# Optimization experiments

Hardware: AMD Instinct MI355X
Metric: run time of the kernel (lower is better)

Reference implementation:

```python
import jax, jax.numpy as jnp
import numpy as np
import math

B, L, C = 8, 1024, 256
H, CH = 8, 32  # num_heads, c_hidden; H*CH == C


def setup_inputs() -> dict:
    key = jax.random.key(0)
    ks = jax.random.split(key, 8)
    s = 0.02
    return {
        "q_x": jax.random.normal(ks[0], (B, L, C), jnp.float32),
        "bias_mask": jnp.zeros((B, 1, 1, L), jnp.float32),
        "bias_pair": jax.random.normal(ks[1], (B, H, L, L), jnp.float32),
        "Wq": jax.random.normal(ks[2], (C, H * CH), jnp.float32) * s,
        "Wk": jax.random.normal(ks[3], (C, H * CH), jnp.float32) * s,
        "Wv": jax.random.normal(ks[4], (C, H * CH), jnp.float32) * s,
        "Wg": jax.random.normal(ks[5], (C, H * CH), jnp.float32) * s,
        "bg": jnp.ones((H * CH,), jnp.float32),  # gating bias init = 1 in AlphaFold
        "Wo": jax.random.normal(ks[6], (H * CH, C), jnp.float32) * s,
        "bo": jnp.zeros((C,), jnp.float32),
    }


def reference(q_x, bias_mask, bias_pair, Wq, Wk, Wv, Wg, bg, Wo, bo):
    # QKV projections (self-attention: kv_x = q_x), split heads -> [B, H, L, CH]
    def proj(W):
        return (q_x @ W).reshape(B, L, H, CH).transpose(0, 2, 1, 3)

    q = proj(Wq) / math.sqrt(CH)
    k = proj(Wk)
    v = proj(Wv)

    # scores + multi-bias add, stable softmax over keys
    a = jnp.einsum("bhqc,bhkc->bhqk", q, k) + bias_mask + bias_pair
    a = jax.nn.softmax(a, axis=-1)

    # weighted values -> [B, L, H, CH]
    o = jnp.einsum("bhqk,bhkc->bhqc", a, v).transpose(0, 2, 1, 3)

    # sigmoid gating from query data
    g = jax.nn.sigmoid(q_x @ Wg + bg).reshape(B, L, H, CH)
    o = o * g

    # merge heads and output projection
    o = o.reshape(B, L, H * CH)
    return o @ Wo + bo
```

## Files before the change

kernel.cpp:

```cpp
#include <hip/hip_runtime.h>
#include <hip/hip_bf16.h>
#include <hip/hip_fp16.h>
#include <math.h>

#define BB 8
#define LL 1024
#define CC 256
#define HH 8
#define CHD 32

typedef __attribute__((ext_vector_type(8))) _Float16 half8;
typedef __attribute__((ext_vector_type(4))) float f32x4;
typedef __attribute__((ext_vector_type(4))) unsigned int u32x4;

__device__ __forceinline__ float u2f(unsigned short u) {
    return __uint_as_float(((unsigned)u) << 16);
}

__device__ __forceinline__ float ldv(const void* p, size_t i, bool f32) {
    return f32 ? ((const float*)p)[i] : u2f(((const unsigned short*)p)[i]);
}
__device__ __forceinline__ float4 ldv4(const void* p, size_t i, bool f32) {
    if (f32) return *(const float4*)((const float*)p + i);
    ushort4 u = *(const ushort4*)((const unsigned short*)p + i);
    return make_float4(u2f(u.x), u2f(u.y), u2f(u.z), u2f(u.w));
}
__device__ __forceinline__ bool probe_f32(const void* bg) {
    return *(const unsigned*)bg == 0x3F800000u;
}

__device__ __forceinline__ unsigned pack_h2(float a, float b) {
    __half2 h = __floats2half2_rn(a, b);
    return *(unsigned*)&h;
}

__global__ __launch_bounds__(256) void proj_kernel(
    const void* __restrict__ qx,
    const void* __restrict__ Wq, const void* __restrict__ Wk,
    const void* __restrict__ Wv, const void* __restrict__ Wg,
    const void* __restrict__ bg,
    __half* __restrict__ q_ws, __half* __restrict__ k_ws,
    __half* __restrict__ vt_ws, __half* __restrict__ g_ws)
{
    const bool f32 = probe_f32(bg);
    __shared__ __align__(16) float xs[16][256];
    const int t  = threadIdx.x;
    const int r0 = blockIdx.x * 16;

    {
        float4* dst = (float4*)(&xs[0][0]);
        for (int i = t; i < 1024; i += 256)
            dst[i] = ldv4(qx, (size_t)r0 * CC + (size_t)i * 4, f32);
    }
    __syncthreads();

    const int mat = t >> 6;
    const int c0  = (t & 63) << 2;
    const void* W = (mat == 0) ? Wq : (mat == 1) ? Wk : (mat == 2) ? Wv : Wg;

    float acc[16][4];
#pragma unroll
    for (int r = 0; r < 16; ++r)
#pragma unroll
        for (int j = 0; j < 4; ++j) acc[r][j] = 0.f;

    for (int kc = 0; kc < 64; ++kc) {
        float4 w[4];
#pragma unroll
        for (int i = 0; i < 4; ++i)
            w[i] = ldv4(W, (size_t)(4 * kc + i) * 256 + c0, f32);
#pragma unroll
        for (int r = 0; r < 16; ++r) {
            float4 x4 = *(const float4*)(&xs[r][kc * 4]);
            acc[r][0] += x4.x * w[0].x + x4.y * w[1].x + x4.z * w[2].x + x4.w * w[3].x;
            acc[r][1] += x4.x * w[0].y + x4.y * w[1].y + x4.z * w[2].y + x4.w * w[3].y;
            acc[r][2] += x4.x * w[0].z + x4.y * w[1].z + x4.z * w[2].z + x4.w * w[3].z;
            acc[r][3] += x4.x * w[0].w + x4.y * w[1].w + x4.z * w[2].w + x4.w * w[3].w;
        }
    }

    if (mat == 3) {
        float bgv[4];
#pragma unroll
        for (int j = 0; j < 4; ++j) bgv[j] = ldv(bg, c0 + j, f32);
#pragma unroll
        for (int r = 0; r < 16; ++r) {
            const int row = r0 + r;
#pragma unroll
            for (int j = 0; j < 4; ++j) {
                float z = acc[r][j] + bgv[j];
                float g = 1.f / (1.f + __expf(-z));
                g_ws[(size_t)row * 256 + c0 + j] = __float2half(g);
            }
        }
    } else if (mat == 2) {
        const int bI = r0 >> 10, l0 = r0 & 1023;
#pragma unroll
        for (int j = 0; j < 4; ++j) {
            const int col = c0 + j, hh = col >> 5, ch = col & 31;
            __half* dst = vt_ws + ((size_t)(bI * HH + hh) * CHD + ch) * LL + l0;
            unsigned p[8];
#pragma unroll
            for (int u = 0; u < 8; ++u)
                p[u] = pack_h2(acc[2 * u][j], acc[2 * u + 1][j]);
            u32x4 w0 = {p[0], p[1], p[2], p[3]};
            u32x4 w1 = {p[4], p[5], p[6], p[7]};
            *(u32x4*)dst = w0;
            *((u32x4*)dst + 1) = w1;
        }
    } else {
        const float scale = (mat == 0) ? 0.17677669529663687f : 1.f;
        __half* dst = (mat == 0) ? q_ws : k_ws;
#pragma unroll
        for (int r = 0; r < 16; ++r) {
            const int row = r0 + r;
            const int b = row >> 10, l = row & 1023;
#pragma unroll
            for (int j = 0; j < 4; ++j) {
                const int col = c0 + j;
                const int h = col >> 5, ch = col & 31;
                dst[((size_t)(b * HH + h) * LL + l) * CHD + ch] =
                    __float2half(acc[r][j] * scale);
            }
        }
    }
}

__global__ __launch_bounds__(256) void attn_mfma_kernel(
    const __half* __restrict__ q_ws, const __half* __restrict__ k_ws,
    const __half* __restrict__ vt_ws, const __half* __restrict__ g_ws,
    const void* __restrict__ mask, const void* __restrict__ bias,
    const void* __restrict__ bg,
    float* __restrict__ og_out)
{
    const bool f32 = probe_f32(bg);
    const int t  = threadIdx.x;
    const int wv = t >> 6;
    const int ln = t & 63;
    const int lq = ln & 15;
    const int g  = ln >> 4;
    const int bh = blockIdx.y;
    const int b  = bh >> 3, h = bh & 7;
    const int q0 = blockIdx.x * 64 + wv * 16;
    const int qi = q0 + lq;

    const half8 qfrag = *(const half8*)(q_ws + ((size_t)bh * LL + qi) * CHD + 8 * g);

    f32x4 o0 = {0.f, 0.f, 0.f, 0.f};
    f32x4 o1 = {0.f, 0.f, 0.f, 0.f};
    float m_run = -1e30f, l_run = 0.f;

    const size_t bias_base = ((size_t)bh * LL + qi) * LL;
    const size_t mask_base = (size_t)b * LL;
    const f32x4 zz = {0.f, 0.f, 0.f, 0.f};

    for (int k0 = 0; k0 < LL; k0 += 64) {
        f32x4 sc[4];
#pragma unroll
        for (int s = 0; s < 4; ++s) {
            half8 kf = *(const half8*)(k_ws +
                ((size_t)bh * LL + k0 + 16 * s + lq) * CHD + 8 * g);
            sc[s] = __builtin_amdgcn_mfma_f32_16x16x32_f16(kf, qfrag, zz, 0, 0, 0);
        }
#pragma unroll
        for (int s = 0; s < 4; ++s) {
            const int kk = k0 + 16 * s + 4 * g;
            float4 b4 = ldv4(bias, bias_base + kk, f32);
            float4 m4 = ldv4(mask, mask_base + kk, f32);
            sc[s].x += b4.x + m4.x;
            sc[s].y += b4.y + m4.y;
            sc[s].z += b4.z + m4.z;
            sc[s].w += b4.w + m4.w;
        }
        float mt = fmaxf(fmaxf(sc[0].x, sc[0].y), fmaxf(sc[0].z, sc[0].w));
#pragma unroll
        for (int s = 1; s < 4; ++s)
            mt = fmaxf(mt, fmaxf(fmaxf(sc[s].x, sc[s].y), fmaxf(sc[s].z, sc[s].w)));
        mt = fmaxf(mt, __shfl_xor(mt, 16));
        mt = fmaxf(mt, __shfl_xor(mt, 32));
        const float mn = fmaxf(m_run, mt);
        const float alpha = __expf(m_run - mn);
        m_run = mn;
        float ls = 0.f;
#pragma unroll
        for (int s = 0; s < 4; ++s) {
            sc[s].x = __expf(sc[s].x - mn); ls += sc[s].x;
            sc[s].y = __expf(sc[s].y - mn); ls += sc[s].y;
            sc[s].z = __expf(sc[s].z - mn); ls += sc[s].z;
            sc[s].w = __expf(sc[s].w - mn); ls += sc[s].w;
        }
        ls += __shfl_xor(ls, 16);
        ls += __shfl_xor(ls, 32);
        l_run = l_run * alpha + ls;
        o0 = o0 * alpha;
        o1 = o1 * alpha;

        unsigned ph[4][2];
#pragma unroll
        for (int s = 0; s < 4; ++s) {
            ph[s][0] = pack_h2(sc[s].x, sc[s].y);
            ph[s][1] = pack_h2(sc[s].z, sc[s].w);
        }
#pragma unroll
        for (int tt = 0; tt < 2; ++tt) {
            unsigned bfr[4];
#pragma unroll
            for (int w = 0; w < 4; ++w) {
                const int src = lq + 16 * (2 * (g & 1) + (w >> 1));
                unsigned lo = (unsigned)__shfl((int)ph[2 * tt + 0][w & 1], src);
                unsigned hi = (unsigned)__shfl((int)ph[2 * tt + 1][w & 1], src);
                bfr[w] = (g >= 2) ? hi : lo;
            }
            u32x4 bv = {bfr[0], bfr[1], bfr[2], bfr[3]};
            half8 pB = __builtin_bit_cast(half8, bv);
            half8 vf0 = *(const half8*)(vt_ws +
                ((size_t)bh * CHD + lq) * LL + k0 + 32 * tt + 8 * g);
            o0 = __builtin_amdgcn_mfma_f32_16x16x32_f16(vf0, pB, o0, 0, 0, 0);
            half8 vf1 = *(const half8*)(vt_ws +
                ((size_t)bh * CHD + 16 + lq) * LL + k0 + 32 * tt + 8 * g);
            o1 = __builtin_amdgcn_mfma_f32_16x16x32_f16(vf1, pB, o1, 0, 0, 0);
        }
    }

    const float inv = 1.f / l_run;
    const size_t row = (size_t)b * LL + qi;
    const __half* gp = g_ws + row * CC + h * CHD + 4 * g;
    float* op = og_out + row * CC + h * CHD + 4 * g;
    float4 r0, r1;
    r0.x = o0.x * inv * __half2float(gp[0]);
    r0.y = o0.y * inv * __half2float(gp[1]);
    r0.z = o0.z * inv * __half2float(gp[2]);
    r0.w = o0.w * inv * __half2float(gp[3]);
    r1.x = o1.x * inv * __half2float(gp[16]);
    r1.y = o1.y * inv * __half2float(gp[17]);
    r1.z = o1.z * inv * __half2float(gp[18]);
    r1.w = o1.w * inv * __half2float(gp[19]);
    *(float4*)op = r0;
    *(float4*)(op + 16) = r1;
}

__global__ __launch_bounds__(256) void out_kernel(
    float* __restrict__ io,
    const void* __restrict__ Wo, const void* __restrict__ bo,
    const void* __restrict__ bg)
{
    const bool f32 = probe_f32(bg);
    __shared__ __align__(16) float xs[16][256];
    const int t  = threadIdx.x;
    const int r0 = blockIdx.x * 16;
    {
        const float4* src = (const float4*)(io + (size_t)r0 * CC);
        float4* dst = (float4*)(&xs[0][0]);
        for (int i = t; i < 1024; i += 256) dst[i] = src[i];
    }
    __syncthreads();

    float acc[16];
#pragma unroll
    for (int r = 0; r < 16; ++r) acc[r] = 0.f;

    for (int kc = 0; kc < 64; ++kc) {
        const float w0 = ldv(Wo, (size_t)(4 * kc + 0) * 256 + t, f32);
        const float w1 = ldv(Wo, (size_t)(4 * kc + 1) * 256 + t, f32);
        const float w2 = ldv(Wo, (size_t)(4 * kc + 2) * 256 + t, f32);
        const float w3 = ldv(Wo, (size_t)(4 * kc + 3) * 256 + t, f32);
#pragma unroll
        for (int r = 0; r < 16; ++r) {
            float4 x4 = *(const float4*)(&xs[r][kc * 4]);
            acc[r] += x4.x * w0 + x4.y * w1 + x4.z * w2 + x4.w * w3;
        }
    }
    const float bov = ldv(bo, t, f32);
#pragma unroll
    for (int r = 0; r < 16; ++r)
        io[(size_t)(r0 + r) * CC + t] = acc[r] + bov;
}

extern "C" void kernel_launch(void* const* d_in, const int* in_sizes, int n_in,
                              void* d_out, int out_size, void* d_ws, size_t ws_size,
                              hipStream_t stream) {
    const void* qx   = d_in[0];
    const void* mask = d_in[1];
    const void* bias = d_in[2];
    const void* Wq   = d_in[3];
    const void* Wk   = d_in[4];
    const void* Wv   = d_in[5];
    const void* Wg   = d_in[6];
    const void* bg   = d_in[7];
    const void* Wo   = d_in[8];
    const void* bo   = d_in[9];
    float* out = (float*)d_out;

    char* ws = (char*)d_ws;
    const size_t TEN = (size_t)BB * LL * CC * sizeof(__half);
    __half* q_ws  = (__half*)(ws + 0 * TEN);
    __half* k_ws  = (__half*)(ws + 1 * TEN);
    __half* vt_ws = (__half*)(ws + 2 * TEN);
    __half* g_ws  = (__half*)(ws + 3 * TEN);

    proj_kernel<<<dim3(512), 256, 0, stream>>>(qx, Wq, Wk, Wv, Wg, bg,
                                               q_ws, k_ws, vt_ws, g_ws);
    attn_mfma_kernel<<<dim3(16, 64), 256, 0, stream>>>(q_ws, k_ws, vt_ws, g_ws,
                                                       mask, bias, bg, out);
    out_kernel<<<dim3(512), 256, 0, stream>>>(out, Wo, bo, bg);
}
```

Baseline: 546.0 us.

## Move QKVG and output projections onto fp16 MFMA with hi/lo split precision

```diff
diff --git a/kernel.cpp b/kernel.cpp
--- a/kernel.cpp
+++ b/kernel.cpp
@@ -13,10 +13,13 @@
 typedef __attribute__((ext_vector_type(4))) float f32x4;
 typedef __attribute__((ext_vector_type(4))) unsigned int u32x4;
 
+#define MFMA16 __builtin_amdgcn_mfma_f32_16x16x32_f16
+#define LO_SCALE 2048.f
+#define LO_INV   4.8828125e-4f
+
 __device__ __forceinline__ float u2f(unsigned short u) {
     return __uint_as_float(((unsigned)u) << 16);
 }
-
 __device__ __forceinline__ float ldv(const void* p, size_t i, bool f32) {
     return f32 ? ((const float*)p)[i] : u2f(((const unsigned short*)p)[i]);
 }
@@ -28,100 +31,148 @@
 __device__ __forceinline__ bool probe_f32(const void* bg) {
     return *(const unsigned*)bg == 0x3F800000u;
 }
-
 __device__ __forceinline__ unsigned pack_h2(float a, float b) {
     __half2 h = __floats2half2_rn(a, b);
     return *(unsigned*)&h;
 }
-
-__global__ __launch_bounds__(256) void proj_kernel(
-    const void* __restrict__ qx,
+__device__ __forceinline__ void store_h4(__half* p, float a, float b, float c, float d) {
+    uint2 u = make_uint2(pack_h2(a, b), pack_h2(c, d));
+    *(uint2*)p = u;
+}
+__device__ __forceinline__ void cvt_store_hilo(__half* ph, __half* pl, float4 v) {
+    __half2 a = __floats2half2_rn(v.x, v.y), b2 = __floats2half2_rn(v.z, v.w);
+    *(uint2*)ph = make_uint2(*(unsigned*)&a, *(unsigned*)&b2);
+    float rx = (v.x - __low2float(a))  * LO_SCALE;
+    float ry = (v.y - __high2float(a)) * LO_SCALE;
+    float rz = (v.z - __low2float(b2)) * LO_SCALE;
+    float rw = (v.w - __high2float(b2)) * LO_SCALE;
+    __half2 c = __floats2half2_rn(rx, ry), d = __floats2half2_rn(rz, rw);
+    *(uint2*)pl = make_uint2(*(unsigned*)&c, *(unsigned*)&d);
+}
+
+__global__ __launch_bounds__(256) void prep_w_kernel(
     const void* __restrict__ Wq, const void* __restrict__ Wk,
     const void* __restrict__ Wv, const void* __restrict__ Wg,
+    const void* __restrict__ Wo, const void* __restrict__ bg,
+    __half* __restrict__ wt_hi, __half* __restrict__ wt_lo)
+{
+    const bool f32 = probe_f32(bg);
+    const int blk = blockIdx.x;
+    const int mi = blk >> 6, tile = blk & 63;
+    const void* W = (mi == 0) ? Wq : (mi == 1) ? Wk : (mi == 2) ? Wv
+                  : (mi == 3) ? Wg : Wo;
+    const int tr = tile >> 3, tc = tile & 7;
+    __shared__ float ts[32][33];
+    const int t = threadIdx.x;
+    for (int e = t; e < 1024; e += 256) {
+        const int r = e >> 5, c = e & 31;
+        ts[r][c] = ldv(W, (size_t)(32 * tr + r) * 256 + 32 * tc + c, f32);
+    }
+    __syncthreads();
+    for (int e = t; e < 1024; e += 256) {
+        const int r = e >> 5, c = e & 31;
+        const float v = ts[c][r];
+        const __half h = __float2half(v);
+        const __half l = __float2half((v - __half2float(h)) * LO_SCALE);
+        const size_t o = (size_t)mi * 65536 + (size_t)(32 * tc + r) * 256 + 32 * tr + c;
+        wt_hi[o] = h;
+        wt_lo[o] = l;
+    }
+}
+
+__global__ __launch_bounds__(256) void proj_mfma_kernel(
+    const void* __restrict__ qx,
+    const __half* __restrict__ wt_hi, const __half* __restrict__ wt_lo,
     const void* __restrict__ bg,
     __half* __restrict__ q_ws, __half* __restrict__ k_ws,
     __half* __restrict__ vt_ws, __half* __restrict__ g_ws)
 {
     const bool f32 = probe_f32(bg);
-    __shared__ __align__(16) float xs[16][256];
+    __shared__ __align__(16) __half xhi[16][264];
+    __shared__ __align__(16) __half xlo[16][264];
     const int t  = threadIdx.x;
-    const int r0 = blockIdx.x * 16;
-
-    {
-        float4* dst = (float4*)(&xs[0][0]);
-        for (int i = t; i < 1024; i += 256)
-            dst[i] = ldv4(qx, (size_t)r0 * CC + (size_t)i * 4, f32);
+    const int m0 = blockIdx.x * 16;
+
+    for (int e = t; e < 1024; e += 256) {
+        const int r = e >> 6, c4 = e & 63;
+        float4 v = ldv4(qx, (size_t)(m0 + r) * CC + (size_t)c4 * 4, f32);
+        cvt_store_hilo(&xhi[r][c4 * 4], &xlo[r][c4 * 4], v);
     }
     __syncthreads();
 
-    const int mat = t >> 6;
-    const int c0  = (t & 63) << 2;
-    const void* W = (mat == 0) ? Wq : (mat == 1) ? Wk : (mat == 2) ? Wv : Wg;
-
-    float acc[16][4];
-#pragma unroll
-    for (int r = 0; r < 16; ++r)
-#pragma unroll
-        for (int j = 0; j < 4; ++j) acc[r][j] = 0.f;
-
-    for (int kc = 0; kc < 64; ++kc) {
-        float4 w[4];
-#pragma unroll
-        for (int i = 0; i < 4; ++i)
-            w[i] = ldv4(W, (size_t)(4 * kc + i) * 256 + c0, f32);
-#pragma unroll
-        for (int r = 0; r < 16; ++r) {
-            float4 x4 = *(const float4*)(&xs[r][kc * 4]);
-            acc[r][0] += x4.x * w[0].x + x4.y * w[1].x + x4.z * w[2].x + x4.w * w[3].x;
-            acc[r][1] += x4.x * w[0].y + x4.y * w[1].y + x4.z * w[2].y + x4.w * w[3].y;
-            acc[r][2] += x4.x * w[0].z + x4.y * w[1].z + x4.z * w[2].z + x4.w * w[3].z;
-            acc[r][3] += x4.x * w[0].w + x4.y * w[1].w + x4.z * w[2].w + x4.w * w[3].w;
-        }
-    }
+    const int ln = t & 63, mat = t >> 6;
+    const int lq = ln & 15, g = ln >> 4;
+    const __half* bh_base = wt_hi + (size_t)mat * 65536 + (size_t)lq * 256 + 8 * g;
+    const __half* bl_base = wt_lo + (size_t)mat * 65536 + (size_t)lq * 256 + 8 * g;
+
+    f32x4 accm[16], accc[16];
+#pragma unroll
+    for (int nt = 0; nt < 16; ++nt) {
+        accm[nt] = (f32x4){0.f, 0.f, 0.f, 0.f};
+        accc[nt] = (f32x4){0.f, 0.f, 0.f, 0.f};
+    }
+
+    const bool vmat = (mat == 2);
+    for (int kc = 0; kc < 8; ++kc) {
+        const half8 ah = *(const half8*)&xhi[lq][kc * 32 + 8 * g];
+        const half8 al = *(const half8*)&xlo[lq][kc * 32 + 8 * g];
+#pragma unroll
+        for (int nt = 0; nt < 16; ++nt) {
+            const half8 bh = *(const half8*)(bh_base + nt * 4096 + kc * 32);
+            const half8 bl = *(const half8*)(bl_base + nt * 4096 + kc * 32);
+            if (!vmat) {
+                accm[nt] = MFMA16(bh, ah, accm[nt], 0, 0, 0);
+                accc[nt] = MFMA16(bl, ah, accc[nt], 0, 0, 0);
+                accc[nt] = MFMA16(bh, al, accc[nt], 0, 0, 0);
+            } else {
+                accm[nt] = MFMA16(ah, bh, accm[nt], 0, 0, 0);
+                accc[nt] = MFMA16(al, bh, accc[nt], 0, 0, 0);
+                accc[nt] = MFMA16(ah, bl, accc[nt], 0, 0, 0);
+            }
+        }
+    }
+
+    const int b  = m0 >> 10;
+    const int l0 = m0 & 1023;
 
     if (mat == 3) {
-        float bgv[4];
-#pragma unroll
-        for (int j = 0; j < 4; ++j) bgv[j] = ldv(bg, c0 + j, f32);
-#pragma unroll
-        for (int r = 0; r < 16; ++r) {
-            const int row = r0 + r;
-#pragma unroll
-            for (int j = 0; j < 4; ++j) {
-                float z = acc[r][j] + bgv[j];
-                float g = 1.f / (1.f + __expf(-z));
-                g_ws[(size_t)row * 256 + c0 + j] = __float2half(g);
-            }
-        }
-    } else if (mat == 2) {
-        const int bI = r0 >> 10, l0 = r0 & 1023;
-#pragma unroll
-        for (int j = 0; j < 4; ++j) {
-            const int col = c0 + j, hh = col >> 5, ch = col & 31;
-            __half* dst = vt_ws + ((size_t)(bI * HH + hh) * CHD + ch) * LL + l0;
-            unsigned p[8];
-#pragma unroll
-            for (int u = 0; u < 8; ++u)
-                p[u] = pack_h2(acc[2 * u][j], acc[2 * u + 1][j]);
-            u32x4 w0 = {p[0], p[1], p[2], p[3]};
-            u32x4 w1 = {p[4], p[5], p[6], p[7]};
-            *(u32x4*)dst = w0;
-            *((u32x4*)dst + 1) = w1;
+        const int m = m0 + lq;
+#pragma unroll
+        for (int nt = 0; nt < 16; ++nt) {
+            const int n0 = nt * 16 + 4 * g;
+            float4 bgv = ldv4(bg, n0, f32);
+            float z0 = accm[nt].x + accc[nt].x * LO_INV + bgv.x;
+            float z1 = accm[nt].y + accc[nt].y * LO_INV + bgv.y;
+            float z2 = accm[nt].z + accc[nt].z * LO_INV + bgv.z;
+            float z3 = accm[nt].w + accc[nt].w * LO_INV + bgv.w;
+            store_h4(g_ws + (size_t)m * 256 + n0,
+                     1.f / (1.f + __expf(-z0)), 1.f / (1.f + __expf(-z1)),
+                     1.f / (1.f + __expf(-z2)), 1.f / (1.f + __expf(-z3)));
+        }
+    } else if (vmat) {
+#pragma unroll
+        for (int nt = 0; nt < 16; ++nt) {
+            const int n = nt * 16 + lq, h = n >> 5, ch = n & 31;
+            __half* dst = vt_ws + ((size_t)(b * HH + h) * CHD + ch) * LL + l0 + 4 * g;
+            store_h4(dst,
+                     accm[nt].x + accc[nt].x * LO_INV,
+                     accm[nt].y + accc[nt].y * LO_INV,
+                     accm[nt].z + accc[nt].z * LO_INV,
+                     accm[nt].w + accc[nt].w * LO_INV);
         }
     } else {
         const float scale = (mat == 0) ? 0.17677669529663687f : 1.f;
-        __half* dst = (mat == 0) ? q_ws : k_ws;
-#pragma unroll
-        for (int r = 0; r < 16; ++r) {
-            const int row = r0 + r;
-            const int b = row >> 10, l = row & 1023;
-#pragma unroll
-            for (int j = 0; j < 4; ++j) {
-                const int col = c0 + j;
-                const int h = col >> 5, ch = col & 31;
-                dst[((size_t)(b * HH + h) * LL + l) * CHD + ch] =
-                    __float2half(acc[r][j] * scale);
-            }
+        __half* dst0 = (mat == 0) ? q_ws : k_ws;
+        const int l = l0 + lq;
+#pragma unroll
+        for (int nt = 0; nt < 16; ++nt) {
+            const int n0 = nt * 16 + 4 * g, h = n0 >> 5, ch = n0 & 31;
+            __half* dst = dst0 + ((size_t)(b * HH + h) * LL + l) * CHD + ch;
+            store_h4(dst,
+                     (accm[nt].x + accc[nt].x * LO_INV) * scale,
+                     (accm[nt].y + accc[nt].y * LO_INV) * scale,
+                     (accm[nt].z + accc[nt].z * LO_INV) * scale,
+                     (accm[nt].w + accc[nt].w * LO_INV) * scale);
         }
     }
 }
@@ -160,7 +211,7 @@
         for (int s = 0; s < 4; ++s) {
             half8 kf = *(const half8*)(k_ws +
                 ((size_t)bh * LL + k0 + 16 * s + lq) * CHD + 8 * g);
-            sc[s] = __builtin_amdgcn_mfma_f32_16x16x32_f16(kf, qfrag, zz, 0, 0, 0);
+            sc[s] = MFMA16(kf, qfrag, zz, 0, 0, 0);
         }
 #pragma unroll
         for (int s = 0; s < 4; ++s) {
@@ -215,10 +266,10 @@
             half8 pB = __builtin_bit_cast(half8, bv);
             half8 vf0 = *(const half8*)(vt_ws +
                 ((size_t)bh * CHD + lq) * LL + k0 + 32 * tt + 8 * g);
-            o0 = __builtin_amdgcn_mfma_f32_16x16x32_f16(vf0, pB, o0, 0, 0, 0);
+            o0 = MFMA16(vf0, pB, o0, 0, 0, 0);
             half8 vf1 = *(const half8*)(vt_ws +
                 ((size_t)bh * CHD + 16 + lq) * LL + k0 + 32 * tt + 8 * g);
-            o1 = __builtin_amdgcn_mfma_f32_16x16x32_f16(vf1, pB, o1, 0, 0, 0);
+            o1 = MFMA16(vf1, pB, o1, 0, 0, 0);
         }
     }
 
@@ -239,41 +290,62 @@
     *(float4*)(op + 16) = r1;
 }
 
-__global__ __launch_bounds__(256) void out_kernel(
+__global__ __launch_bounds__(256) void out_mfma_kernel(
     float* __restrict__ io,
-    const void* __restrict__ Wo, const void* __restrict__ bo,
-    const void* __restrict__ bg)
+    const __half* __restrict__ wt_hi, const __half* __restrict__ wt_lo,
+    const void* __restrict__ bo, const void* __restrict__ bg)
 {
     const bool f32 = probe_f32(bg);
-    __shared__ __align__(16) float xs[16][256];
+    __shared__ __align__(16) __half xhi[16][264];
+    __shared__ __align__(16) __half xlo[16][264];
     const int t  = threadIdx.x;
-    const int r0 = blockIdx.x * 16;
-    {
-        const float4* src = (const float4*)(io + (size_t)r0 * CC);
-        float4* dst = (float4*)(&xs[0][0]);
-        for (int i = t; i < 1024; i += 256) dst[i] = src[i];
+    const int m0 = blockIdx.x * 16;
+
+    for (int e = t; e < 1024; e += 256) {
+        const int r = e >> 6, c4 = e & 63;
+        float4 v = *(const float4*)(io + (size_t)(m0 + r) * CC + (size_t)c4 * 4);
+        cvt_store_hilo(&xhi[r][c4 * 4], &xlo[r][c4 * 4], v);
     }
     __syncthreads();
 
-    float acc[16];
-#pragma unroll
-    for (int r = 0; r < 16; ++r) acc[r] = 0.f;
-
-    for (int kc = 0; kc < 64; ++kc) {
-        const float w0 = ldv(Wo, (size_t)(4 * kc + 0) * 256 + t, f32);
-        const float w1 = ldv(Wo, (size_t)(4 * kc + 1) * 256 + t, f32);
-        const float w2 = ldv(Wo, (size_t)(4 * kc + 2) * 256 + t, f32);
-        const float w3 = ldv(Wo, (size_t)(4 * kc + 3) * 256 + t, f32);
-#pragma unroll
-        for (int r = 0; r < 16; ++r) {
-            float4 x4 = *(const float4*)(&xs[r][kc * 4]);
-            acc[r] += x4.x * w0 + x4.y * w1 + x4.z * w2 + x4.w * w3;
-        }
-    }
-    const float bov = ldv(bo, t, f32);
-#pragma unroll
-    for (int r = 0; r < 16; ++r)
-        io[(size_t)(r0 + r) * CC + t] = acc[r] + bov;
+    const int ln = t & 63, wv = t >> 6;
+    const int lq = ln & 15, g = ln >> 4;
+    const __half* bh_base = wt_hi + (size_t)4 * 65536 + (size_t)lq * 256 + 8 * g;
+    const __half* bl_base = wt_lo + (size_t)4 * 65536 + (size_t)lq * 256 + 8 * g;
+
+    f32x4 accm[4], accc[4];
+#pragma unroll
+    for (int j = 0; j < 4; ++j) {
+        accm[j] = (f32x4){0.f, 0.f, 0.f, 0.f};
+        accc[j] = (f32x4){0.f, 0.f, 0.f, 0.f};
+    }
+
+    for (int kc = 0; kc < 8; ++kc) {
+        const half8 ah = *(const half8*)&xhi[lq][kc * 32 + 8 * g];
+        const half8 al = *(const half8*)&xlo[lq][kc * 32 + 8 * g];
+#pragma unroll
+        for (int j = 0; j < 4; ++j) {
+            const int nt = wv * 4 + j;
+            const half8 bh = *(const half8*)(bh_base + nt * 4096 + kc * 32);
+            const half8 bl = *(const half8*)(bl_base + nt * 4096 + kc * 32);
+            accm[j] = MFMA16(bh, ah, accm[j], 0, 0, 0);
+            accc[j] = MFMA16(bl, ah, accc[j], 0, 0, 0);
+            accc[j] = MFMA16(bh, al, accc[j], 0, 0, 0);
+        }
+    }
+
+    const int m = m0 + lq;
+#pragma unroll
+    for (int j = 0; j < 4; ++j) {
+        const int n0 = (wv * 4 + j) * 16 + 4 * g;
+        float4 bov = ldv4(bo, n0, f32);
+        float4 r;
+        r.x = accm[j].x + accc[j].x * LO_INV + bov.x;
+        r.y = accm[j].y + accc[j].y * LO_INV + bov.y;
+        r.z = accm[j].z + accc[j].z * LO_INV + bov.z;
+        r.w = accm[j].w + accc[j].w * LO_INV + bov.w;
+        *(float4*)(io + (size_t)m * 256 + n0) = r;
+    }
 }
 
 extern "C" void kernel_launch(void* const* d_in, const int* in_sizes, int n_in,
@@ -297,10 +369,14 @@
     __half* k_ws  = (__half*)(ws + 1 * TEN);
     __half* vt_ws = (__half*)(ws + 2 * TEN);
     __half* g_ws  = (__half*)(ws + 3 * TEN);
-
-    proj_kernel<<<dim3(512), 256, 0, stream>>>(qx, Wq, Wk, Wv, Wg, bg,
-                                               q_ws, k_ws, vt_ws, g_ws);
+    __half* wt_hi = (__half*)(ws + 4 * TEN);
+    __half* wt_lo = (__half*)(ws + 4 * TEN + (size_t)2 * 1024 * 1024);
+
+    prep_w_kernel<<<dim3(320), 256, 0, stream>>>(Wq, Wk, Wv, Wg, Wo, bg,
+                                                 wt_hi, wt_lo);
+    proj_mfma_kernel<<<dim3(512), 256, 0, stream>>>(qx, wt_hi, wt_lo, bg,
+                                                    q_ws, k_ws, vt_ws, g_ws);
     attn_mfma_kernel<<<dim3(16, 64), 256, 0, stream>>>(q_ws, k_ws, vt_ws, g_ws,
                                                        mask, bias, bg, out);
-    out_kernel<<<dim3(512), 256, 0, stream>>>(out, Wo, bo, bg);
-}
+    out_mfma_kernel<<<dim3(512), 256, 0, stream>>>(out, wt_hi, wt_lo, bo, bg);
+}
```

New measurement: 519.6 us. 1.05x faster.
